# Kernel tuning notes

Measured on AMD Instinct MI355X. Metric: run time of the kernel, lower is better.

## Reference

```python
import jax, jax.numpy as jnp
import numpy as np

B, T, C = 2, 2048, 1024
H = 16
HD = C // H  # head_size = 64


def setup_inputs() -> dict:
    key = jax.random.key(0)
    k1, k2, k3 = jax.random.split(key, 3)
    x = jax.random.normal(k1, (B, T, C), dtype=jnp.float32)
    W_qkv = jax.random.normal(k2, (C, 3 * C), dtype=jnp.float32) * (1.0 / np.sqrt(C))
    b_qkv = jnp.zeros((3 * C,), dtype=jnp.float32)
    W_proj = jax.random.normal(k3, (C, C), dtype=jnp.float32) * (1.0 / np.sqrt(C))
    b_proj = jnp.zeros((C,), dtype=jnp.float32)
    return {"x": x, "W_qkv": W_qkv, "b_qkv": b_qkv, "W_proj": W_proj, "b_proj": b_proj}


def reference(x, W_qkv, b_qkv, W_proj, b_proj):
    Bc, Tc, Cc = x.shape
    qkv = x @ W_qkv + b_qkv                      # [B,T,3C]
    # Faithful to torch: view(B,T,H,3*HD) then chunk(3,-1) -> per-head interleaved split
    qkv = qkv.reshape(Bc, Tc, H, 3 * HD)
    q = qkv[..., 0 * HD:1 * HD]                  # [B,T,H,HD]
    k = qkv[..., 1 * HD:2 * HD]
    v = qkv[..., 2 * HD:3 * HD]
    # scores: [B,H,T,T]
    att = jnp.einsum('bqhd,bkhd->bhqk', q, k) / np.sqrt(HD)
    causal = jnp.tril(jnp.ones((Tc, Tc), dtype=bool))
    att = jnp.where(causal[None, None, :, :], att, -jnp.inf)
    att = jax.nn.softmax(att, axis=-1)
    out = jnp.einsum('bhqk,bkhd->bqhd', att, v).reshape(Bc, Tc, Cc)
    return out @ W_proj + b_proj
```

## Files before the change

kernel.cpp:

```cpp
#include <hip/hip_runtime.h>
#include <hip/hip_bf16.h>
#include <stdint.h>
#include <math.h>

#define T_SEQ 2048
#define NHEAD 16
#define CDIM 1024
#define QKV2_LD 2048

typedef __attribute__((ext_vector_type(8))) short short8;
typedef __attribute__((ext_vector_type(4))) short short4v;
typedef __attribute__((ext_vector_type(4))) float floatx4;
typedef __attribute__((ext_vector_type(2))) unsigned int uint2v;
typedef __attribute__((ext_vector_type(4))) unsigned int uint4v;

static __device__ __forceinline__ short bf16b(float f) {
    __hip_bfloat16 h = __float2bfloat16(f);
    return __builtin_bit_cast(short, h);
}

__device__ __forceinline__ void transpose_body(
    const float* __restrict__ in, __hip_bfloat16* __restrict__ out,
    int R, int C, int bx, int by, int tid)
{
    __shared__ short tile[64][65];
    const int r0 = by << 6;
    const int c0 = bx << 6;
    #pragma unroll
    for (int t = 0; t < 4; ++t) {
        int ch = t * 256 + tid;
        int rr = ch >> 4, cc = (ch & 15) << 2;
        float4 v = *(const float4*)(in + (size_t)(r0 + rr) * C + c0 + cc);
        tile[rr][cc + 0] = bf16b(v.x);
        tile[rr][cc + 1] = bf16b(v.y);
        tile[rr][cc + 2] = bf16b(v.z);
        tile[rr][cc + 3] = bf16b(v.w);
    }
    __syncthreads();
    #pragma unroll
    for (int t = 0; t < 2; ++t) {
        int ch = t * 256 + tid;
        int cc = ch >> 3, rr8 = (ch & 7) << 3;
        short8 v;
        #pragma unroll
        for (int j = 0; j < 8; ++j) v[j] = tile[rr8 + j][cc];
        *(short8*)(out + (size_t)(c0 + cc) * R + r0 + rr8) = v;
    }
}

__global__ __launch_bounds__(256) void prep_kernel(
    const float* __restrict__ x,     __hip_bfloat16* __restrict__ xb,
    const float* __restrict__ Wqkv,  __hip_bfloat16* __restrict__ WqkvT,
    const float* __restrict__ Wproj, __hip_bfloat16* __restrict__ WprojT)
{
    const int bid = blockIdx.x;
    const int tid = threadIdx.x;
    if (bid < 2048) {
        int i = (bid * 256 + tid) * 8;
        float4 a = *(const float4*)(x + i);
        float4 b = *(const float4*)(x + i + 4);
        short8 o;
        o[0] = bf16b(a.x); o[1] = bf16b(a.y); o[2] = bf16b(a.z); o[3] = bf16b(a.w);
        o[4] = bf16b(b.x); o[5] = bf16b(b.y); o[6] = bf16b(b.z); o[7] = bf16b(b.w);
        *(short8*)(xb + i) = o;
    } else if (bid < 2816) {
        int r = bid - 2048;
        transpose_body(Wqkv, WqkvT, 1024, 3072, r % 48, r / 48, tid);
    } else {
        int r = bid - 2816;
        transpose_body(Wproj, WprojT, 1024, 1024, r & 15, r >> 4, tid);
    }
}

template <int MI, int NI, int MINW, bool QKV, typename OutT>
__global__ __launch_bounds__(256, MINW) void gemm_bias_kernel(
    const __hip_bfloat16* __restrict__ A,
    const __hip_bfloat16* __restrict__ Bt,
    const float* __restrict__ bias,
    OutT* __restrict__ C,
    __hip_bfloat16* __restrict__ vT,
    int M, int N, int K)
{
    __shared__ short As[MI * 32 * 64];
    __shared__ short Bs[NI * 32 * 64];
    const int tid  = threadIdx.x;
    const int lane = tid & 63;
    const int w    = tid >> 6;
    const int quad = lane >> 4;
    const int c16  = lane & 15;
    const int m0 = blockIdx.x * (MI * 32);
    const int n0 = blockIdx.y * (NI * 32);
    const int wm = (w >> 1) * (MI * 16);
    const int wn = (w & 1) * (NI * 16);

    floatx4 acc[MI][NI] = {};

    for (int kt = 0; kt < K; kt += 64) {
        __syncthreads();
        #pragma unroll
        for (int r = 0; r < MI; ++r) {
            int ch = r * 256 + tid;
            int row = ch >> 3, k8 = (ch & 7) << 3;
            const __hip_bfloat16* ga = A + (size_t)(m0 + row) * K + kt + k8;
            __builtin_amdgcn_global_load_lds(
                (const __attribute__((address_space(1))) void*)ga,
                (__attribute__((address_space(3))) void*)&As[ch * 8], 16, 0, 0);
        }
        #pragma unroll
        for (int r = 0; r < NI; ++r) {
            int ch = r * 256 + tid;
            int row = ch >> 3, k8 = (ch & 7) << 3;
            const __hip_bfloat16* gb = Bt + (size_t)(n0 + row) * K + kt + k8;
            __builtin_amdgcn_global_load_lds(
                (const __attribute__((address_space(1))) void*)gb,
                (__attribute__((address_space(3))) void*)&Bs[ch * 8], 16, 0, 0);
        }
        __syncthreads();
        #pragma unroll
        for (int ko = 0; ko < 64; ko += 32) {
            short8 af[MI], bfr[NI];
            #pragma unroll
            for (int mi = 0; mi < MI; ++mi)
                af[mi] = *(const short8*)&As[(wm + mi * 16 + c16) * 64 + ko + quad * 8];
            #pragma unroll
            for (int ni = 0; ni < NI; ++ni)
                bfr[ni] = *(const short8*)&Bs[(wn + ni * 16 + c16) * 64 + ko + quad * 8];
            #pragma unroll
            for (int mi = 0; mi < MI; ++mi)
                #pragma unroll
                for (int ni = 0; ni < NI; ++ni)
                    acc[mi][ni] = __builtin_amdgcn_mfma_f32_16x16x32_bf16(
                        af[mi], bfr[ni], acc[mi][ni], 0, 0, 0);
        }
    }

    if constexpr (QKV) {
        const int colblk = (n0 + wn) >> 6;
        const int head = colblk / 3;
        const int kind = colblk % 3;
        const int b    = m0 >> 11;
        __syncthreads();
        if (kind == 2) {
            short* tp = (w < 2) ? &As[w * 4096] : &Bs[(w - 2) * 4096];
            #pragma unroll
            for (int mi = 0; mi < MI; ++mi)
                #pragma unroll
                for (int ni = 0; ni < NI; ++ni) {
                    int hd = ni * 16 + c16;
                    float bv = bias[n0 + wn + hd];
                    short4v pk;
                    #pragma unroll
                    for (int r2 = 0; r2 < 4; ++r2) pk[r2] = bf16b(acc[mi][ni][r2] + bv);
                    int tc = mi * 4 + quad;
                    *(short4v*)&tp[hd * 64 + ((tc ^ ((hd & 7) << 1)) << 2)] = pk;
                }
            const size_t vb2 = ((size_t)(b * 16 + head)) * 64 * T_SEQ;
            const int t0 = (m0 + wm) & 2047;
            #pragma unroll
            for (int it = 0; it < 8; ++it) {
                int hd = it * 8 + (lane >> 3);
                int tc2 = (lane & 7) << 1;
                short8 vv = *(const short8*)&tp[hd * 64 + ((tc2 ^ ((hd & 7) << 1)) << 2)];
                *(short8*)(vT + vb2 + (size_t)hd * T_SEQ + t0 + ((lane & 7) << 3)) = vv;
            }
        } else {
            const int cbase = head * 128 + kind * 64;
            const float qsc = (kind == 0) ? 0.18033688011112042f : 1.0f;
            #pragma unroll
            for (int mi = 0; mi < MI; ++mi)
                #pragma unroll
                for (int ni = 0; ni < NI; ++ni) {
                    float bv = bias[n0 + wn + ni * 16 + c16];
                    int col = cbase + ni * 16 + c16;
                    #pragma unroll
                    for (int r2 = 0; r2 < 4; ++r2) {
                        int row = m0 + wm + mi * 16 + quad * 4 + r2;
                        C[(size_t)row * QKV2_LD + col] =
                            __float2bfloat16((acc[mi][ni][r2] + bv) * qsc);
                    }
                }
        }
    } else {
        #pragma unroll
        for (int mi = 0; mi < MI; ++mi)
            #pragma unroll
            for (int ni = 0; ni < NI; ++ni) {
                int col = n0 + wn + ni * 16 + c16;
                float bv = bias[col];
                #pragma unroll
                for (int r2 = 0; r2 < 4; ++r2) {
                    int row = m0 + wm + mi * 16 + quad * 4 + r2;
                    float v = acc[mi][ni][r2] + bv;
                    if constexpr (__is_same(OutT, float)) {
                        C[(size_t)row * N + col] = v;
                    } else {
                        C[(size_t)row * N + col] = __float2bfloat16(v);
                    }
                }
            }
    }
}

__global__ __launch_bounds__(512, 4) void attn_kernel(
    const __hip_bfloat16* __restrict__ qkv,
    const __hip_bfloat16* __restrict__ vT,
    __hip_bfloat16* __restrict__ attn_out)
{
    __shared__ short Ks[2][64 * 64];
    __shared__ short Vs[2][64 * 64];

    const int hb = blockIdx.x;
    const int yj = blockIdx.y & 7, yk = blockIdx.y >> 3;
    const int qb = yk ? (15 - yj) : yj;
    const int h  = hb & 15;
    const int b  = hb >> 4;
    const int tid  = threadIdx.x;
    const int lane = tid & 63;
    const int w    = tid >> 6;
    const int quad = lane >> 4;
    const int c16  = lane & 15;

    const size_t rowbase = (size_t)b * T_SEQ;
    const size_t vbase   = (size_t)hb * 64 * T_SEQ;
    const int q0   = qb << 7;
    const int wrow = w << 4;
    const int hoff = h * 128;
    const int key  = c16 & 7;
    const int dt   = (q0 + wrow) >> 6;
    const int mrow = ((w & 3) << 4) + c16;
    const int nkt  = (qb << 1) + 2;

    short8 qf[2];
    #pragma unroll
    for (int ko = 0; ko < 2; ++ko)
        qf[ko] = *(const short8*)(qkv +
            (rowbase + q0 + wrow + c16) * QKV2_LD + hoff + ko * 32 + quad * 8);

    floatx4 O[4] = {};
    floatx4 lp4 = {};

    auto stage = [&](int kt, int bsel) {
        const int k0s = kt << 6;
        {
            int ch = tid;
            int krow = ch >> 3;
            int hc = (ch & 7) ^ (krow & 7);
            const __hip_bfloat16* g = qkv + (rowbase + k0s + krow) * QKV2_LD + hoff + 64 + hc * 8;
            __builtin_amdgcn_global_load_lds(
                (const __attribute__((address_space(1))) void*)g,
                (__attribute__((address_space(3))) void*)&Ks[bsel][ch * 8], 16, 0, 0);
        }
        {
            int ch = tid;
            int hd = ch >> 3;
            int kc = (ch & 7) ^ (hd & 7);
            const __hip_bfloat16* g = vT + vbase + (size_t)hd * T_SEQ + k0s + kc * 8;
            __builtin_amdgcn_global_load_lds(
                (const __attribute__((address_space(1))) void*)g,
                (__attribute__((address_space(3))) void*)&Vs[bsel][ch * 8], 16, 0, 0);
        }
    };

    stage(0, 0);
    int buf = 0;

    for (int kt = 0; kt < nkt; ++kt) {
        __syncthreads();
        if (kt + 1 < nkt) stage(kt + 1, buf ^ 1);

        if (kt <= dt) {
            short8 kf[2][4];
            #pragma unroll
            for (int ko = 0; ko < 2; ++ko)
                #pragma unroll
                for (int ni = 0; ni < 4; ++ni) {
                    int sl = ((4 * ko + quad) ^ key) << 3;
                    kf[ko][ni] = *(const short8*)&Ks[buf][(ni * 16 + c16) * 64 + sl];
                }

            floatx4 S[4] = {};
            __builtin_amdgcn_s_setprio(1);
            #pragma unroll
            for (int ko = 0; ko < 2; ++ko)
                #pragma unroll
                for (int ni = 0; ni < 4; ++ni)
                    S[ni] = __builtin_amdgcn_mfma_f32_16x16x32_bf16(
                        kf[ko][ni], qf[ko], S[ni], 0, 0, 0);
            __builtin_amdgcn_s_setprio(0);

            short8 vb[2][4];
            #pragma unroll
            for (int ko = 0; ko < 2; ++ko)
                #pragma unroll
                for (int ni = 0; ni < 4; ++ni) {
                    int sl = ((4 * ko + quad) ^ key) << 3;
                    vb[ko][ni] = *(const short8*)&Vs[buf][(ni * 16 + c16) * 64 + sl];
                }

            if (kt == dt) {
                #pragma unroll
                for (int ni = 0; ni < 4; ++ni)
                    #pragma unroll
                    for (int r = 0; r < 4; ++r) {
                        bool msk = (ni * 16 + quad * 4 + r) > mrow;
                        float pe = msk ? 0.f : exp2f(S[ni][r]);
                        S[ni][r] = pe;
                        lp4[r] += pe;
                    }
            } else {
                #pragma unroll
                for (int ni = 0; ni < 4; ++ni)
                    #pragma unroll
                    for (int r = 0; r < 4; ++r) {
                        float pe = exp2f(S[ni][r]);
                        S[ni][r] = pe;
                        lp4[r] += pe;
                    }
            }

            unsigned pw[4][2];
            #pragma unroll
            for (int ni = 0; ni < 4; ++ni) {
                asm("v_cvt_pk_bf16_f32 %0, %1, %2"
                    : "=v"(pw[ni][0]) : "v"(S[ni][0]), "v"(S[ni][1]));
                asm("v_cvt_pk_bf16_f32 %0, %1, %2"
                    : "=v"(pw[ni][1]) : "v"(S[ni][2]), "v"(S[ni][3]));
            }

            #pragma unroll
            for (int ko = 0; ko < 2; ++ko) {
                uint4v pb;
                uint2v t0 = __builtin_amdgcn_permlane32_swap(pw[2 * ko][0], pw[2 * ko + 1][0], false, false);
                uint2v u0 = __builtin_amdgcn_permlane16_swap(t0[0], t0[1], false, false);
                uint2v t1 = __builtin_amdgcn_permlane32_swap(pw[2 * ko][1], pw[2 * ko + 1][1], false, false);
                uint2v u1 = __builtin_amdgcn_permlane16_swap(t1[0], t1[1], false, false);
                pb[0] = u0[0]; pb[2] = u0[1];
                pb[1] = u1[0]; pb[3] = u1[1];
                short8 pa = __builtin_bit_cast(short8, pb);
                __builtin_amdgcn_s_setprio(1);
                #pragma unroll
                for (int ni = 0; ni < 4; ++ni)
                    O[ni] = __builtin_amdgcn_mfma_f32_16x16x32_bf16(
                        vb[ko][ni], pa, O[ni], 0, 0, 0);
                __builtin_amdgcn_s_setprio(0);
            }
        }
        buf ^= 1;
    }

    float l = lp4[0] + lp4[1] + lp4[2] + lp4[3];
    l += __shfl_xor(l, 16);
    l += __shfl_xor(l, 32);
    float inv = 1.0f / l;
    size_t row = rowbase + q0 + wrow + c16;
    #pragma unroll
    for (int ni = 0; ni < 4; ++ni) {
        short4v o;
        #pragma unroll
        for (int r = 0; r < 4; ++r) o[r] = bf16b(O[ni][r] * inv);
        *(short4v*)(attn_out + row * CDIM + h * 64 + ni * 16 + quad * 4) = o;
    }
}

extern "C" void kernel_launch(void* const* d_in, const int* in_sizes, int n_in,
                              void* d_out, int out_size, void* d_ws, size_t ws_size,
                              hipStream_t stream) {
    const float* x     = (const float*)d_in[0];
    const float* Wqkv  = (const float*)d_in[1];
    const float* bqkv  = (const float*)d_in[2];
    const float* Wproj = (const float*)d_in[3];
    const float* bproj = (const float*)d_in[4];
    float* out = (float*)d_out;

    __hip_bfloat16* xb     = (__hip_bfloat16*)d_ws;
    __hip_bfloat16* WqkvT  = xb     + (size_t)4096 * 1024;
    __hip_bfloat16* WprojT = WqkvT  + (size_t)3072 * 1024;
    __hip_bfloat16* qkv2   = WprojT + (size_t)1024 * 1024;
    __hip_bfloat16* vT     = qkv2   + (size_t)4096 * 2048;
    __hip_bfloat16* attn   = vT     + (size_t)32 * 64 * 2048;

    prep_kernel<<<3072, 256, 0, stream>>>(x, xb, Wqkv, WqkvT, Wproj, WprojT);
    gemm_bias_kernel<4, 4, 2, true, __hip_bfloat16>
        <<<dim3(4096 / 128, 3072 / 128), 256, 0, stream>>>(
        xb, WqkvT, bqkv, qkv2, vT, 4096, 3072, 1024);
    attn_kernel<<<dim3(32, 16), 512, 0, stream>>>(qkv2, vT, attn);
    gemm_bias_kernel<2, 2, 4, false, float>
        <<<dim3(4096 / 64, 1024 / 64), 256, 0, stream>>>(
        attn, WprojT, bproj, out, nullptr, 4096, 1024, 1024);
}
```

Measured before the change: 182.2 us.

## Process two 16-row query groups per wave in attention, halving block threads

The attention kernel now runs 4 waves per block instead of 8. Each wave handles 32 query rows as two 16-row groups and reuses each K and V fragment read from LDS for both groups' MFMAs. The aim is to halve LDS fragment reads per query row and raise MFMA density per wave. In exchange it roughly doubles accumulator registers, may reduce occupancy, and coarsens causal-skip granularity to 32 rows, so some fully masked work is done.

Result: slower. 220.7 us (+21.1%).

```diff
diff --git a/kernel.cpp b/kernel.cpp
--- a/kernel.cpp
+++ b/kernel.cpp
@@ -201,7 +201,7 @@
     }
 }
 
-__global__ __launch_bounds__(512, 4) void attn_kernel(
+__global__ __launch_bounds__(256, 4) void attn_kernel(
     const __hip_bfloat16* __restrict__ qkv,
     const __hip_bfloat16* __restrict__ vT,
     __hip_bfloat16* __restrict__ attn_out)
@@ -223,26 +223,28 @@
     const size_t rowbase = (size_t)b * T_SEQ;
     const size_t vbase   = (size_t)hb * 64 * T_SEQ;
     const int q0   = qb << 7;
-    const int wrow = w << 4;
     const int hoff = h * 128;
     const int key  = c16 & 7;
-    const int dt   = (q0 + wrow) >> 6;
-    const int mrow = ((w & 3) << 4) + c16;
+    const int dtw  = (qb << 1) + (w >> 1);
+    const int lb   = (w & 1) << 5;
     const int nkt  = (qb << 1) + 2;
 
-    short8 qf[2];
+    short8 qf[2][2];
     #pragma unroll
-    for (int ko = 0; ko < 2; ++ko)
-        qf[ko] = *(const short8*)(qkv +
-            (rowbase + q0 + wrow + c16) * QKV2_LD + hoff + ko * 32 + quad * 8);
-
-    floatx4 O[4] = {};
-    floatx4 lp4 = {};
+    for (int G = 0; G < 2; ++G)
+        #pragma unroll
+        for (int ko = 0; ko < 2; ++ko)
+            qf[G][ko] = *(const short8*)(qkv +
+                (rowbase + q0 + (w << 5) + (G << 4) + c16) * QKV2_LD + hoff + ko * 32 + quad * 8);
+
+    floatx4 OA[4] = {}, OB[4] = {};
+    floatx4 lpA = {}, lpB = {};
 
     auto stage = [&](int kt, int bsel) {
         const int k0s = kt << 6;
-        {
-            int ch = tid;
+        #pragma unroll
+        for (int r = 0; r < 2; ++r) {
+            int ch = r * 256 + tid;
             int krow = ch >> 3;
             int hc = (ch & 7) ^ (krow & 7);
             const __hip_bfloat16* g = qkv + (rowbase + k0s + krow) * QKV2_LD + hoff + 64 + hc * 8;
@@ -250,8 +252,9 @@
                 (const __attribute__((address_space(1))) void*)g,
                 (__attribute__((address_space(3))) void*)&Ks[bsel][ch * 8], 16, 0, 0);
         }
-        {
-            int ch = tid;
+        #pragma unroll
+        for (int r = 0; r < 2; ++r) {
+            int ch = r * 256 + tid;
             int hd = ch >> 3;
             int kc = (ch & 7) ^ (hd & 7);
             const __hip_bfloat16* g = vT + vbase + (size_t)hd * T_SEQ + k0s + kc * 8;
@@ -268,97 +271,125 @@
         __syncthreads();
         if (kt + 1 < nkt) stage(kt + 1, buf ^ 1);
 
-        if (kt <= dt) {
-            short8 kf[2][4];
-            #pragma unroll
-            for (int ko = 0; ko < 2; ++ko)
+        if (kt <= dtw) {
+            floatx4 SA[4] = {}, SB[4] = {};
+            #pragma unroll
+            for (int ko = 0; ko < 2; ++ko) {
+                short8 kf[4];
                 #pragma unroll
                 for (int ni = 0; ni < 4; ++ni) {
                     int sl = ((4 * ko + quad) ^ key) << 3;
-                    kf[ko][ni] = *(const short8*)&Ks[buf][(ni * 16 + c16) * 64 + sl];
-                }
-
-            floatx4 S[4] = {};
-            __builtin_amdgcn_s_setprio(1);
-            #pragma unroll
-            for (int ko = 0; ko < 2; ++ko)
-                #pragma unroll
-                for (int ni = 0; ni < 4; ++ni)
-                    S[ni] = __builtin_amdgcn_mfma_f32_16x16x32_bf16(
-                        kf[ko][ni], qf[ko], S[ni], 0, 0, 0);
-            __builtin_amdgcn_s_setprio(0);
-
-            short8 vb[2][4];
-            #pragma unroll
-            for (int ko = 0; ko < 2; ++ko)
+                    kf[ni] = *(const short8*)&Ks[buf][(ni * 16 + c16) * 64 + sl];
+                }
+                __builtin_amdgcn_s_setprio(1);
+                #pragma unroll
+                for (int ni = 0; ni < 4; ++ni)
+                    SA[ni] = __builtin_amdgcn_mfma_f32_16x16x32_bf16(
+                        kf[ni], qf[0][ko], SA[ni], 0, 0, 0);
+                #pragma unroll
+                for (int ni = 0; ni < 4; ++ni)
+                    SB[ni] = __builtin_amdgcn_mfma_f32_16x16x32_bf16(
+                        kf[ni], qf[1][ko], SB[ni], 0, 0, 0);
+                __builtin_amdgcn_s_setprio(0);
+            }
+
+            if (kt == dtw) {
+                #pragma unroll
+                for (int ni = 0; ni < 4; ++ni)
+                    #pragma unroll
+                    for (int r = 0; r < 4; ++r) {
+                        int keyi = ni * 16 + quad * 4 + r;
+                        float pa2 = (keyi > (lb + c16))      ? 0.f : exp2f(SA[ni][r]);
+                        float pb2 = (keyi > (lb + 16 + c16)) ? 0.f : exp2f(SB[ni][r]);
+                        SA[ni][r] = pa2; lpA[r] += pa2;
+                        SB[ni][r] = pb2; lpB[r] += pb2;
+                    }
+            } else {
+                #pragma unroll
+                for (int ni = 0; ni < 4; ++ni)
+                    #pragma unroll
+                    for (int r = 0; r < 4; ++r) {
+                        float pa2 = exp2f(SA[ni][r]);
+                        float pb2 = exp2f(SB[ni][r]);
+                        SA[ni][r] = pa2; lpA[r] += pa2;
+                        SB[ni][r] = pb2; lpB[r] += pb2;
+                    }
+            }
+
+            unsigned pwA[4][2], pwB[4][2];
+            #pragma unroll
+            for (int ni = 0; ni < 4; ++ni) {
+                asm("v_cvt_pk_bf16_f32 %0, %1, %2" : "=v"(pwA[ni][0]) : "v"(SA[ni][0]), "v"(SA[ni][1]));
+                asm("v_cvt_pk_bf16_f32 %0, %1, %2" : "=v"(pwA[ni][1]) : "v"(SA[ni][2]), "v"(SA[ni][3]));
+                asm("v_cvt_pk_bf16_f32 %0, %1, %2" : "=v"(pwB[ni][0]) : "v"(SB[ni][0]), "v"(SB[ni][1]));
+                asm("v_cvt_pk_bf16_f32 %0, %1, %2" : "=v"(pwB[ni][1]) : "v"(SB[ni][2]), "v"(SB[ni][3]));
+            }
+
+            #pragma unroll
+            for (int ko = 0; ko < 2; ++ko) {
+                short8 vb[4];
                 #pragma unroll
                 for (int ni = 0; ni < 4; ++ni) {
                     int sl = ((4 * ko + quad) ^ key) << 3;
-                    vb[ko][ni] = *(const short8*)&Vs[buf][(ni * 16 + c16) * 64 + sl];
-                }
-
-            if (kt == dt) {
-                #pragma unroll
-                for (int ni = 0; ni < 4; ++ni)
-                    #pragma unroll
-                    for (int r = 0; r < 4; ++r) {
-                        bool msk = (ni * 16 + quad * 4 + r) > mrow;
-                        float pe = msk ? 0.f : exp2f(S[ni][r]);
-                        S[ni][r] = pe;
-                        lp4[r] += pe;
-                    }
-            } else {
-                #pragma unroll
-                for (int ni = 0; ni < 4; ++ni)
-                    #pragma unroll
-                    for (int r = 0; r < 4; ++r) {
-                        float pe = exp2f(S[ni][r]);
-                        S[ni][r] = pe;
-                        lp4[r] += pe;
-                    }
-            }
-
-            unsigned pw[4][2];
-            #pragma unroll
-            for (int ni = 0; ni < 4; ++ni) {
-                asm("v_cvt_pk_bf16_f32 %0, %1, %2"
-                    : "=v"(pw[ni][0]) : "v"(S[ni][0]), "v"(S[ni][1]));
-                asm("v_cvt_pk_bf16_f32 %0, %1, %2"
-                    : "=v"(pw[ni][1]) : "v"(S[ni][2]), "v"(S[ni][3]));
-            }
-
-            #pragma unroll
-            for (int ko = 0; ko < 2; ++ko) {
-                uint4v pb;
-                uint2v t0 = __builtin_amdgcn_permlane32_swap(pw[2 * ko][0], pw[2 * ko + 1][0], false, false);
-                uint2v u0 = __builtin_amdgcn_permlane16_swap(t0[0], t0[1], false, false);
-                uint2v t1 = __builtin_amdgcn_permlane32_swap(pw[2 * ko][1], pw[2 * ko + 1][1], false, false);
-                uint2v u1 = __builtin_amdgcn_permlane16_swap(t1[0], t1[1], false, false);
-                pb[0] = u0[0]; pb[2] = u0[1];
-                pb[1] = u1[0]; pb[3] = u1[1];
-                short8 pa = __builtin_bit_cast(short8, pb);
+                    vb[ni] = *(const short8*)&Vs[buf][(ni * 16 + c16) * 64 + sl];
+                }
+                uint4v pbA, pbB;
+                {
+                    uint2v t0 = __builtin_amdgcn_permlane32_swap(pwA[2 * ko][0], pwA[2 * ko + 1][0], false, false);
+                    uint2v u0 = __builtin_amdgcn_permlane16_swap(t0[0], t0[1], false, false);
+                    uint2v t1 = __builtin_amdgcn_permlane32_swap(pwA[2 * ko][1], pwA[2 * ko + 1][1], false, false);
+                    uint2v u1 = __builtin_amdgcn_permlane16_swap(t1[0], t1[1], false, false);
+                    pbA[0] = u0[0]; pbA[2] = u0[1]; pbA[1] = u1[0]; pbA[3] = u1[1];
+                }
+                {
+                    uint2v t0 = __builtin_amdgcn_permlane32_swap(pwB[2 * ko][0], pwB[2 * ko + 1][0], false, false);
+                    uint2v u0 = __builtin_amdgcn_permlane16_swap(t0[0], t0[1], false, false);
+                    uint2v t1 = __builtin_amdgcn_permlane32_swap(pwB[2 * ko][1], pwB[2 * ko + 1][1], false, false);
+                    uint2v u1 = __builtin_amdgcn_permlane16_swap(t1[0], t1[1], false, false);
+                    pbB[0] = u0[0]; pbB[2] = u0[1]; pbB[1] = u1[0]; pbB[3] = u1[1];
+                }
+                short8 paA = __builtin_bit_cast(short8, pbA);
+                short8 paB = __builtin_bit_cast(short8, pbB);
                 __builtin_amdgcn_s_setprio(1);
                 #pragma unroll
                 for (int ni = 0; ni < 4; ++ni)
-                    O[ni] = __builtin_amdgcn_mfma_f32_16x16x32_bf16(
-                        vb[ko][ni], pa, O[ni], 0, 0, 0);
+                    OA[ni] = __builtin_amdgcn_mfma_f32_16x16x32_bf16(vb[ni], paA, OA[ni], 0, 0, 0);
+                #pragma unroll
+                for (int ni = 0; ni < 4; ++ni)
+                    OB[ni] = __builtin_amdgcn_mfma_f32_16x16x32_bf16(vb[ni], paB, OB[ni], 0, 0, 0);
                 __builtin_amdgcn_s_setprio(0);
             }
         }
         buf ^= 1;
     }
 
-    float l = lp4[0] + lp4[1] + lp4[2] + lp4[3];
-    l += __shfl_xor(l, 16);
-    l += __shfl_xor(l, 32);
-    float inv = 1.0f / l;
-    size_t row = rowbase + q0 + wrow + c16;
-    #pragma unroll
-    for (int ni = 0; ni < 4; ++ni) {
-        short4v o;
-        #pragma unroll
-        for (int r = 0; r < 4; ++r) o[r] = bf16b(O[ni][r] * inv);
-        *(short4v*)(attn_out + row * CDIM + h * 64 + ni * 16 + quad * 4) = o;
+    {
+        float l = lpA[0] + lpA[1] + lpA[2] + lpA[3];
+        l += __shfl_xor(l, 16);
+        l += __shfl_xor(l, 32);
+        float inv = 1.0f / l;
+        size_t row = rowbase + q0 + (w << 5) + c16;
+        #pragma unroll
+        for (int ni = 0; ni < 4; ++ni) {
+            short4v o;
+            #pragma unroll
+            for (int r = 0; r < 4; ++r) o[r] = bf16b(OA[ni][r] * inv);
+            *(short4v*)(attn_out + row * CDIM + h * 64 + ni * 16 + quad * 4) = o;
+        }
+    }
+    {
+        float l = lpB[0] + lpB[1] + lpB[2] + lpB[3];
+        l += __shfl_xor(l, 16);
+        l += __shfl_xor(l, 32);
+        float inv = 1.0f / l;
+        size_t row = rowbase + q0 + (w << 5) + 16 + c16;
+        #pragma unroll
+        for (int ni = 0; ni < 4; ++ni) {
+            short4v o;
+            #pragma unroll
+            for (int r = 0; r < 4; ++r) o[r] = bf16b(OB[ni][r] * inv);
+            *(short4v*)(attn_out + row * CDIM + h * 64 + ni * 16 + quad * 4) = o;
+        }
     }
 }
 
@@ -383,7 +414,7 @@
     gemm_bias_kernel<4, 4, 2, true, __hip_bfloat16>
         <<<dim3(4096 / 128, 3072 / 128), 256, 0, stream>>>(
         xb, WqkvT, bqkv, qkv2, vT, 4096, 3072, 1024);
-    attn_kernel<<<dim3(32, 16), 512, 0, stream>>>(qkv2, vT, attn);
+    attn_kernel<<<dim3(32, 16), 256, 0, stream>>>(qkv2, vT, attn);
     gemm_bias_kernel<2, 2, 4, false, float>
         <<<dim3(4096 / 64, 1024 / 64), 256, 0, stream>>>(
         attn, WprojT, bproj, out, nullptr, 4096, 1024, 1024);
```
